# Performance work log

Hardware: AMD Instinct MI355X
Metric: run time of the kernel (lower is better)

## Reference

```python
import jax, jax.numpy as jnp
import numpy as np

N_NODES = 100000
N_EDGES = 1600000
D_IN = 64
D_OUT = 64


def _sage_conv(x, Wl, b, Wr, src, dst, inv_deg):
    # mean-aggregate neighbor features: gather x[src], scatter-sum into dst, divide by degree
    agg = jax.ops.segment_sum(x[src], dst, num_segments=N_NODES)  # [N, d]
    agg = agg * inv_deg                                            # mean with deg clamped >= 1
    # PyG SAGEConv: lin_l(agg) (with bias) + lin_r(x) (no bias)
    return agg @ Wl.T + b + x @ Wr.T


def setup_inputs() -> dict:
    key = jax.random.key(0)
    ks = jax.random.split(key, 8)
    x = jax.random.normal(ks[0], (N_NODES, D_IN), dtype=jnp.float32)
    edge_index = jax.random.randint(ks[1], (2, N_EDGES), 0, N_NODES, dtype=jnp.int64)
    s1 = 1.0 / np.sqrt(D_IN)
    s2 = 1.0 / np.sqrt(D_OUT)
    Wl1 = jax.random.uniform(ks[2], (D_OUT, D_IN), jnp.float32, -s1, s1)
    b1 = jnp.zeros((D_OUT,), jnp.float32)
    Wr1 = jax.random.uniform(ks[3], (D_OUT, D_IN), jnp.float32, -s1, s1)
    Wl2 = jax.random.uniform(ks[4], (D_OUT, D_OUT), jnp.float32, -s2, s2)
    b2 = jnp.zeros((D_OUT,), jnp.float32)
    Wr2 = jax.random.uniform(ks[5], (D_OUT, D_OUT), jnp.float32, -s2, s2)
    return {"x": x, "edge_index": edge_index, "Wl1": Wl1, "b1": b1, "Wr1": Wr1,
            "Wl2": Wl2, "b2": b2, "Wr2": Wr2}


def reference(x, edge_index, Wl1, b1, Wr1, Wl2, b2, Wr2):
    src, dst = edge_index[0], edge_index[1]
    deg = jax.ops.segment_sum(jnp.ones((N_EDGES,), jnp.float32), dst, num_segments=N_NODES)
    inv_deg = (1.0 / jnp.maximum(deg, 1.0))[:, None]  # [N, 1]
    h = _sage_conv(x, Wl1, b1, Wr1, src, dst, inv_deg)
    h = _sage_conv(h, Wl2, b2, Wr2, src, dst, inv_deg)
    return h
```

## Files before the change

### kernel.cpp

```cpp
#include <hip/hip_runtime.h>
#include <hip/hip_bf16.h>

#define NN 100000
#define NE 1600000
#define NB 196
#define BCAP 9216
#define BIN_CHUNK 8192
#define BIN_BLKS ((NE + BIN_CHUNK - 1) / BIN_CHUNK)

typedef __attribute__((ext_vector_type(8))) short bf16x8;
typedef __attribute__((ext_vector_type(4))) float f32x4;

__device__ inline unsigned short f2bf(float f) {
    union { __hip_bfloat16 h; unsigned short u; } c;
    c.h = __float2bfloat16(f);
    return c.u;
}

__global__ void k_init(int* __restrict__ gcur) {
    int t = threadIdx.x;
    if (t < NB) gcur[t] = t * BCAP;
}

__global__ void k_wcvt(const float* __restrict__ Wl1, const float* __restrict__ Wr1,
                       const float* __restrict__ Wl2, const float* __restrict__ Wr2,
                       unsigned short* __restrict__ Wc1, unsigned short* __restrict__ Wc2) {
    int e = blockIdx.x * 256 + threadIdx.x;
    if (e < 4096) {
        int fo = e >> 6, k = e & 63;
        Wc1[fo * 128 + k]      = f2bf(Wl1[e]);
        Wc1[fo * 128 + 64 + k] = f2bf(Wr1[e]);
        Wc2[fo * 128 + k]      = f2bf(Wl2[e]);
        Wc2[fo * 128 + 64 + k] = f2bf(Wr2[e]);
    }
}

__global__ __launch_bounds__(256) void k_xcvt(const float* __restrict__ x,
                                              unsigned short* __restrict__ xb) {
    int i = blockIdx.x * 256 + threadIdx.x;
    if (i >= NN * 64 / 8) return;
    const float4* p = (const float4*)(x + (size_t)i * 8);
    float4 v0 = p[0], v1 = p[1];
    union { bf16x8 v; unsigned short u[8]; } c;
    c.u[0] = f2bf(v0.x); c.u[1] = f2bf(v0.y); c.u[2] = f2bf(v0.z); c.u[3] = f2bf(v0.w);
    c.u[4] = f2bf(v1.x); c.u[5] = f2bf(v1.y); c.u[6] = f2bf(v1.z); c.u[7] = f2bf(v1.w);
    *(bf16x8*)(xb + (size_t)i * 8) = c.v;
}

__global__ __launch_bounds__(256) void k_bin(const int* __restrict__ src,
                                             const int* __restrict__ dst,
                                             int* __restrict__ gcur,
                                             unsigned* __restrict__ binned) {
    __shared__ int hist[NB];
    __shared__ int base[NB];
    __shared__ int lcur[NB];
    const int t = threadIdx.x;
    const int e0 = blockIdx.x * BIN_CHUNK;
    const int n = min(BIN_CHUNK, NE - e0);
    for (int i = t; i < NB; i += 256) { hist[i] = 0; lcur[i] = 0; }
    __syncthreads();
    for (int i = t; i < n; i += 256)
        atomicAdd(&hist[dst[e0 + i] >> 9], 1);
    __syncthreads();
    for (int i = t; i < NB; i += 256) {
        int h = hist[i];
        base[i] = h ? atomicAdd(&gcur[i], h) : 0;
    }
    __syncthreads();
    for (int i = t; i < n; i += 256) {
        int d = dst[e0 + i];
        int s = src[e0 + i];
        int b = d >> 9;
        int p = base[b] + atomicAdd(&lcur[b], 1);
        binned[p] = ((unsigned)(d & 511) << 17) | (unsigned)s;
    }
}

__global__ __launch_bounds__(256) void k_csr(const int* __restrict__ gcur,
                                             unsigned* __restrict__ binned,
                                             int2* __restrict__ noff,
                                             float* __restrict__ inv) {
    __shared__ unsigned buf[BCAP];
    __shared__ int h[512];
    __shared__ int off[512];
    __shared__ int lcur[512];
    __shared__ int s[256];
    const int b = blockIdx.x;
    const int t = threadIdx.x;
    const int base = b * BCAP;
    const int cnt = min(gcur[b] - base, BCAP);
    for (int i = t; i < 512; i += 256) h[i] = 0;
    __syncthreads();
    for (int i = t; i < cnt; i += 256) {
        unsigned v = binned[base + i];
        buf[i] = v;
        atomicAdd(&h[v >> 17], 1);
    }
    __syncthreads();
    int a0 = h[2 * t], a1 = h[2 * t + 1];
    s[t] = a0 + a1;
    __syncthreads();
    #pragma unroll
    for (int o = 1; o < 256; o <<= 1) {
        int u = (t >= o) ? s[t - o] : 0;
        __syncthreads();
        s[t] += u;
        __syncthreads();
    }
    int ex = s[t] - (a0 + a1);
    off[2 * t] = ex;          lcur[2 * t] = ex;
    off[2 * t + 1] = ex + a0; lcur[2 * t + 1] = ex + a0;
    __syncthreads();
    for (int i = t; i < cnt; i += 256) {
        unsigned v = buf[i];
        int dl = v >> 17;
        int p = atomicAdd(&lcur[dl], 1);
        binned[base + p] = v & 0x1FFFFu;
    }
    #pragma unroll
    for (int q = 0; q < 2; ++q) {
        int l = 2 * t + q;
        int node = b * 512 + l;
        if (node < NN) {
            int st = base + off[l];
            noff[node] = make_int2(st, st + h[l]);
            inv[node] = 1.0f / fmaxf((float)h[l], 1.0f);
        }
    }
}

__global__ __launch_bounds__(512) void k_agg(const unsigned short* __restrict__ feat,
                                             const int2* __restrict__ noff,
                                             const unsigned* __restrict__ csr,
                                             const float* __restrict__ inv,
                                             unsigned short* __restrict__ A) {
    int gid = (blockIdx.x * 512 + threadIdx.x) >> 3;
    int p = threadIdx.x & 7;
    if (gid >= NN) return;
    int2 oe = noff[gid];
    int beg = oe.x, end = oe.y;
    float a[8] = {0.f, 0.f, 0.f, 0.f, 0.f, 0.f, 0.f, 0.f};

    #define UNPK(uu, k)                                        \
        a[2*(k)]   += __uint_as_float((uu) << 16);             \
        a[2*(k)+1] += __uint_as_float((uu) & 0xffff0000u);

    int j = beg;
    for (; j + 4 <= end; j += 4) {
        unsigned s0 = csr[j], s1 = csr[j + 1], s2 = csr[j + 2], s3 = csr[j + 3];
        uint4 u0 = *(const uint4*)(feat + (size_t)s0 * 64 + p * 8);
        uint4 u1 = *(const uint4*)(feat + (size_t)s1 * 64 + p * 8);
        uint4 u2 = *(const uint4*)(feat + (size_t)s2 * 64 + p * 8);
        uint4 u3 = *(const uint4*)(feat + (size_t)s3 * 64 + p * 8);
        UNPK(u0.x, 0) UNPK(u0.y, 1) UNPK(u0.z, 2) UNPK(u0.w, 3)
        UNPK(u1.x, 0) UNPK(u1.y, 1) UNPK(u1.z, 2) UNPK(u1.w, 3)
        UNPK(u2.x, 0) UNPK(u2.y, 1) UNPK(u2.z, 2) UNPK(u2.w, 3)
        UNPK(u3.x, 0) UNPK(u3.y, 1) UNPK(u3.z, 2) UNPK(u3.w, 3)
    }
    for (; j < end; ++j) {
        uint4 u0 = *(const uint4*)(feat + (size_t)csr[j] * 64 + p * 8);
        UNPK(u0.x, 0) UNPK(u0.y, 1) UNPK(u0.z, 2) UNPK(u0.w, 3)
    }
    #undef UNPK

    float iv = inv[gid];
    union { bf16x8 v; unsigned short u[8]; } c;
    #pragma unroll
    for (int e = 0; e < 8; ++e) c.u[e] = f2bf(a[e] * iv);
    *(bf16x8*)(A + (size_t)gid * 64 + p * 8) = c.v;
}

__global__ __launch_bounds__(256) void k_gemm(const unsigned short* __restrict__ Ab,
                                              const unsigned short* __restrict__ Xb,
                                              const unsigned short* __restrict__ Wc,
                                              const float* __restrict__ bias,
                                              float* __restrict__ Cf,
                                              unsigned short* __restrict__ Cb) {
    const int t = threadIdx.x;
    const int w = t >> 6;
    const int l = t & 63;
    const int cn = l & 15;
    const int ks = l >> 4;
    const int n0 = blockIdx.x * 64 + w * 16;

    int arow = n0 + cn;
    int aclamp = (arow < NN) ? arow : 0;

    f32x4 acc0 = {0.f, 0.f, 0.f, 0.f};
    f32x4 acc1 = {0.f, 0.f, 0.f, 0.f};
    f32x4 acc2 = {0.f, 0.f, 0.f, 0.f};
    f32x4 acc3 = {0.f, 0.f, 0.f, 0.f};

    #pragma unroll
    for (int kb = 0; kb < 4; ++kb) {
        const unsigned short* ap = (kb < 2)
            ? (Ab + (size_t)aclamp * 64 + kb * 32 + ks * 8)
            : (Xb + (size_t)aclamp * 64 + (kb - 2) * 32 + ks * 8);
        bf16x8 aa = *(const bf16x8*)ap;
        const unsigned short* wb = Wc + cn * 128 + kb * 32 + ks * 8;
        bf16x8 b0 = *(const bf16x8*)(wb);
        bf16x8 b1 = *(const bf16x8*)(wb + 16 * 128);
        bf16x8 b2 = *(const bf16x8*)(wb + 32 * 128);
        bf16x8 b3 = *(const bf16x8*)(wb + 48 * 128);
        acc0 = __builtin_amdgcn_mfma_f32_16x16x32_bf16(aa, b0, acc0, 0, 0, 0);
        acc1 = __builtin_amdgcn_mfma_f32_16x16x32_bf16(aa, b1, acc1, 0, 0, 0);
        acc2 = __builtin_amdgcn_mfma_f32_16x16x32_bf16(aa, b2, acc2, 0, 0, 0);
        acc3 = __builtin_amdgcn_mfma_f32_16x16x32_bf16(aa, b3, acc3, 0, 0, 0);
    }

    #pragma unroll
    for (int f = 0; f < 4; ++f) {
        f32x4 av = (f == 0) ? acc0 : (f == 1) ? acc1 : (f == 2) ? acc2 : acc3;
        float bv = bias[f * 16 + cn];
        #pragma unroll
        for (int r = 0; r < 4; ++r) {
            int node = n0 + ks * 4 + r;
            if (node < NN) {
                float val = av[r] + bv;
                if (Cb) Cb[(size_t)node * 64 + f * 16 + cn] = f2bf(val);
                else    Cf[(size_t)node * 64 + f * 16 + cn] = val;
            }
        }
    }
}


extern "C" void kernel_launch(void* const* d_in, const int* in_sizes, int n_in,
                              void* d_out, int out_size, void* d_ws, size_t ws_size,
                              hipStream_t stream) {
    const float* x   = (const float*)d_in[0];
    const int*   ei  = (const int*)d_in[1];
    const int*   src = ei;
    const int*   dst = ei + NE;
    const float* Wl1 = (const float*)d_in[2];
    const float* b1  = (const float*)d_in[3];
    const float* Wr1 = (const float*)d_in[4];
    const float* Wl2 = (const float*)d_in[5];
    const float* b2  = (const float*)d_in[6];
    const float* Wr2 = (const float*)d_in[7];
    float* out = (float*)d_out;

    char* ws = (char*)d_ws;
    size_t off = 0;
    auto alloc = [&](size_t bytes) {
        void* p = ws + off;
        off = (off + bytes + 255) & ~(size_t)255;
        return p;
    };
    unsigned short* A      = (unsigned short*)alloc(2 * (size_t)NN * 64);
    unsigned short* xb     = (unsigned short*)alloc(2 * (size_t)NN * 64);
    unsigned short* h1b    = (unsigned short*)alloc(2 * (size_t)NN * 64);
    unsigned*       binned = (unsigned*)alloc(sizeof(unsigned) * NB * BCAP);
    int2*           noff   = (int2*)alloc(sizeof(int2) * NN);
    float*          inv    = (float*)alloc(sizeof(float) * NN);
    int*            gcur   = (int*)alloc(sizeof(int) * NB);
    unsigned short* Wc1    = (unsigned short*)alloc(2 * 64 * 128);
    unsigned short* Wc2    = (unsigned short*)alloc(2 * 64 * 128);

    k_init<<<1, 256, 0, stream>>>(gcur);
    k_wcvt<<<16, 256, 0, stream>>>(Wl1, Wr1, Wl2, Wr2, Wc1, Wc2);
    k_xcvt<<<(NN * 64 / 8 + 255) / 256, 256, 0, stream>>>(x, xb);
    k_bin <<<BIN_BLKS, 256, 0, stream>>>(src, dst, gcur, binned);
    k_csr <<<NB, 256, 0, stream>>>(gcur, binned, noff, inv);

    k_agg <<<((size_t)NN * 8 + 511) / 512, 512, 0, stream>>>(xb, noff, binned, inv, A);
    k_gemm<<<(NN + 63) / 64, 256, 0, stream>>>(A, xb, Wc1, b1, (float*)nullptr, h1b);

    k_agg <<<((size_t)NN * 8 + 511) / 512, 512, 0, stream>>>(h1b, noff, binned, inv, A);
    k_gemm<<<(NN + 63) / 64, 256, 0, stream>>>(A, h1b, Wc2, b2, out, (unsigned short*)nullptr);
}
```

Measured before the change: 165.4 us.

## Fuse aggregation with GEMM via shared memory and merge prep kernels

Each layer's aggregation and linear transform now run in one kernel. The mean-aggregated tile is written to LDS and fed straight into the MFMA, so the intermediate A buffer no longer makes a global round trip and one launch per layer is saved. The init, weight-convert and x-convert kernels are merged into a single prep kernel. The binning kernel also reads src and dst as int4. The GEMM work is split over 8 waves per 64-node block, each doing two output column groups.

```diff
diff --git a/kernel.cpp b/kernel.cpp
--- a/kernel.cpp
+++ b/kernel.cpp
@@ -17,34 +17,32 @@
     return c.u;
 }
 
-__global__ void k_init(int* __restrict__ gcur) {
-    int t = threadIdx.x;
-    if (t < NB) gcur[t] = t * BCAP;
-}
-
-__global__ void k_wcvt(const float* __restrict__ Wl1, const float* __restrict__ Wr1,
-                       const float* __restrict__ Wl2, const float* __restrict__ Wr2,
-                       unsigned short* __restrict__ Wc1, unsigned short* __restrict__ Wc2) {
-    int e = blockIdx.x * 256 + threadIdx.x;
-    if (e < 4096) {
-        int fo = e >> 6, k = e & 63;
-        Wc1[fo * 128 + k]      = f2bf(Wl1[e]);
-        Wc1[fo * 128 + 64 + k] = f2bf(Wr1[e]);
-        Wc2[fo * 128 + k]      = f2bf(Wl2[e]);
-        Wc2[fo * 128 + 64 + k] = f2bf(Wr2[e]);
-    }
-}
-
-__global__ __launch_bounds__(256) void k_xcvt(const float* __restrict__ x,
-                                              unsigned short* __restrict__ xb) {
+__global__ __launch_bounds__(256) void k_prep(const float* __restrict__ x,
+                                              unsigned short* __restrict__ xb,
+                                              const float* __restrict__ Wl1,
+                                              const float* __restrict__ Wr1,
+                                              const float* __restrict__ Wl2,
+                                              const float* __restrict__ Wr2,
+                                              unsigned short* __restrict__ Wc1,
+                                              unsigned short* __restrict__ Wc2,
+                                              int* __restrict__ gcur) {
     int i = blockIdx.x * 256 + threadIdx.x;
-    if (i >= NN * 64 / 8) return;
-    const float4* p = (const float4*)(x + (size_t)i * 8);
-    float4 v0 = p[0], v1 = p[1];
-    union { bf16x8 v; unsigned short u[8]; } c;
-    c.u[0] = f2bf(v0.x); c.u[1] = f2bf(v0.y); c.u[2] = f2bf(v0.z); c.u[3] = f2bf(v0.w);
-    c.u[4] = f2bf(v1.x); c.u[5] = f2bf(v1.y); c.u[6] = f2bf(v1.z); c.u[7] = f2bf(v1.w);
-    *(bf16x8*)(xb + (size_t)i * 8) = c.v;
+    if (i < NB) gcur[i] = i * BCAP;
+    if (i < 4096) {
+        int fo = i >> 6, k = i & 63;
+        Wc1[fo * 128 + k]      = f2bf(Wl1[i]);
+        Wc1[fo * 128 + 64 + k] = f2bf(Wr1[i]);
+        Wc2[fo * 128 + k]      = f2bf(Wl2[i]);
+        Wc2[fo * 128 + 64 + k] = f2bf(Wr2[i]);
+    }
+    if (i < NN * 64 / 8) {
+        const float4* p = (const float4*)(x + (size_t)i * 8);
+        float4 v0 = p[0], v1 = p[1];
+        union { bf16x8 v; unsigned short u[8]; } c;
+        c.u[0] = f2bf(v0.x); c.u[1] = f2bf(v0.y); c.u[2] = f2bf(v0.z); c.u[3] = f2bf(v0.w);
+        c.u[4] = f2bf(v1.x); c.u[5] = f2bf(v1.y); c.u[6] = f2bf(v1.z); c.u[7] = f2bf(v1.w);
+        *(bf16x8*)(xb + (size_t)i * 8) = c.v;
+    }
 }
 
 __global__ __launch_bounds__(256) void k_bin(const int* __restrict__ src,
@@ -56,23 +54,33 @@
     __shared__ int lcur[NB];
     const int t = threadIdx.x;
     const int e0 = blockIdx.x * BIN_CHUNK;
-    const int n = min(BIN_CHUNK, NE - e0);
+    const int n4 = min(BIN_CHUNK, NE - e0) >> 2;
     for (int i = t; i < NB; i += 256) { hist[i] = 0; lcur[i] = 0; }
     __syncthreads();
-    for (int i = t; i < n; i += 256)
-        atomicAdd(&hist[dst[e0 + i] >> 9], 1);
+    const int4* d4p = (const int4*)(dst + e0);
+    const int4* s4p = (const int4*)(src + e0);
+    for (int i = t; i < n4; i += 256) {
+        int4 d = d4p[i];
+        atomicAdd(&hist[d.x >> 9], 1);
+        atomicAdd(&hist[d.y >> 9], 1);
+        atomicAdd(&hist[d.z >> 9], 1);
+        atomicAdd(&hist[d.w >> 9], 1);
+    }
     __syncthreads();
     for (int i = t; i < NB; i += 256) {
         int h = hist[i];
         base[i] = h ? atomicAdd(&gcur[i], h) : 0;
     }
     __syncthreads();
-    for (int i = t; i < n; i += 256) {
-        int d = dst[e0 + i];
-        int s = src[e0 + i];
-        int b = d >> 9;
-        int p = base[b] + atomicAdd(&lcur[b], 1);
-        binned[p] = ((unsigned)(d & 511) << 17) | (unsigned)s;
+    for (int i = t; i < n4; i += 256) {
+        int4 d = d4p[i];
+        int4 s = s4p[i];
+        #define PLACE(dd, ss) {                                         \
+            int b = (dd) >> 9;                                          \
+            int p = base[b] + atomicAdd(&lcur[b], 1);                   \
+            binned[p] = ((unsigned)((dd) & 511) << 17) | (unsigned)(ss);}
+        PLACE(d.x, s.x) PLACE(d.y, s.y) PLACE(d.z, s.z) PLACE(d.w, s.w)
+        #undef PLACE
     }
 }
 
@@ -129,92 +137,91 @@
     }
 }
 
-__global__ __launch_bounds__(512) void k_agg(const unsigned short* __restrict__ feat,
-                                             const int2* __restrict__ noff,
-                                             const unsigned* __restrict__ csr,
-                                             const float* __restrict__ inv,
-                                             unsigned short* __restrict__ A) {
-    int gid = (blockIdx.x * 512 + threadIdx.x) >> 3;
-    int p = threadIdx.x & 7;
-    if (gid >= NN) return;
-    int2 oe = noff[gid];
-    int beg = oe.x, end = oe.y;
-    float a[8] = {0.f, 0.f, 0.f, 0.f, 0.f, 0.f, 0.f, 0.f};
-
-    #define UNPK(uu, k)                                        \
-        a[2*(k)]   += __uint_as_float((uu) << 16);             \
-        a[2*(k)+1] += __uint_as_float((uu) & 0xffff0000u);
-
-    int j = beg;
-    for (; j + 4 <= end; j += 4) {
-        unsigned s0 = csr[j], s1 = csr[j + 1], s2 = csr[j + 2], s3 = csr[j + 3];
-        uint4 u0 = *(const uint4*)(feat + (size_t)s0 * 64 + p * 8);
-        uint4 u1 = *(const uint4*)(feat + (size_t)s1 * 64 + p * 8);
-        uint4 u2 = *(const uint4*)(feat + (size_t)s2 * 64 + p * 8);
-        uint4 u3 = *(const uint4*)(feat + (size_t)s3 * 64 + p * 8);
-        UNPK(u0.x, 0) UNPK(u0.y, 1) UNPK(u0.z, 2) UNPK(u0.w, 3)
-        UNPK(u1.x, 0) UNPK(u1.y, 1) UNPK(u1.z, 2) UNPK(u1.w, 3)
-        UNPK(u2.x, 0) UNPK(u2.y, 1) UNPK(u2.z, 2) UNPK(u2.w, 3)
-        UNPK(u3.x, 0) UNPK(u3.y, 1) UNPK(u3.z, 2) UNPK(u3.w, 3)
-    }
-    for (; j < end; ++j) {
-        uint4 u0 = *(const uint4*)(feat + (size_t)csr[j] * 64 + p * 8);
-        UNPK(u0.x, 0) UNPK(u0.y, 1) UNPK(u0.z, 2) UNPK(u0.w, 3)
-    }
-    #undef UNPK
-
-    float iv = inv[gid];
-    union { bf16x8 v; unsigned short u[8]; } c;
-    #pragma unroll
-    for (int e = 0; e < 8; ++e) c.u[e] = f2bf(a[e] * iv);
-    *(bf16x8*)(A + (size_t)gid * 64 + p * 8) = c.v;
-}
-
-__global__ __launch_bounds__(256) void k_gemm(const unsigned short* __restrict__ Ab,
-                                              const unsigned short* __restrict__ Xb,
-                                              const unsigned short* __restrict__ Wc,
-                                              const float* __restrict__ bias,
-                                              float* __restrict__ Cf,
-                                              unsigned short* __restrict__ Cb) {
+__global__ __launch_bounds__(512) void k_fused(const unsigned short* __restrict__ feat,
+                                               const int2* __restrict__ noff,
+                                               const unsigned* __restrict__ csr,
+                                               const float* __restrict__ inv,
+                                               const unsigned short* __restrict__ Wc,
+                                               const float* __restrict__ bias,
+                                               float* __restrict__ Cf,
+                                               unsigned short* __restrict__ Cb) {
+    __shared__ unsigned short sA[64 * 72];
     const int t = threadIdx.x;
+    const int n0 = blockIdx.x * 64;
+
+    {
+        const int g = t >> 3;
+        const int p = t & 7;
+        const int node = n0 + g;
+        float a[8] = {0.f, 0.f, 0.f, 0.f, 0.f, 0.f, 0.f, 0.f};
+        float iv = 0.f;
+        if (node < NN) {
+            int2 oe = noff[node];
+            int beg = oe.x, end = oe.y;
+
+            #define UNPK(uu, k)                                        \
+                a[2*(k)]   += __uint_as_float((uu) << 16);             \
+                a[2*(k)+1] += __uint_as_float((uu) & 0xffff0000u);
+
+            int j = beg;
+            for (; j + 4 <= end; j += 4) {
+                unsigned s0 = csr[j], s1 = csr[j + 1], s2 = csr[j + 2], s3 = csr[j + 3];
+                uint4 u0 = *(const uint4*)(feat + (size_t)s0 * 64 + p * 8);
+                uint4 u1 = *(const uint4*)(feat + (size_t)s1 * 64 + p * 8);
+                uint4 u2 = *(const uint4*)(feat + (size_t)s2 * 64 + p * 8);
+                uint4 u3 = *(const uint4*)(feat + (size_t)s3 * 64 + p * 8);
+                UNPK(u0.x, 0) UNPK(u0.y, 1) UNPK(u0.z, 2) UNPK(u0.w, 3)
+                UNPK(u1.x, 0) UNPK(u1.y, 1) UNPK(u1.z, 2) UNPK(u1.w, 3)
+                UNPK(u2.x, 0) UNPK(u2.y, 1) UNPK(u2.z, 2) UNPK(u2.w, 3)
+                UNPK(u3.x, 0) UNPK(u3.y, 1) UNPK(u3.z, 2) UNPK(u3.w, 3)
+            }
+            for (; j < end; ++j) {
+                uint4 u0 = *(const uint4*)(feat + (size_t)csr[j] * 64 + p * 8);
+                UNPK(u0.x, 0) UNPK(u0.y, 1) UNPK(u0.z, 2) UNPK(u0.w, 3)
+            }
+            #undef UNPK
+            iv = inv[node];
+        }
+        union { bf16x8 v; unsigned short u[8]; } c;
+        #pragma unroll
+        for (int e = 0; e < 8; ++e) c.u[e] = f2bf(a[e] * iv);
+        *(bf16x8*)(&sA[g * 72 + p * 8]) = c.v;
+    }
+    __syncthreads();
+
     const int w = t >> 6;
     const int l = t & 63;
     const int cn = l & 15;
     const int ks = l >> 4;
-    const int n0 = blockIdx.x * 64 + w * 16;
-
-    int arow = n0 + cn;
-    int aclamp = (arow < NN) ? arow : 0;
+    const int s = w & 3;
+    const int h = w >> 2;
+    const int lrow = s * 16 + cn;
+    const int arow = n0 + lrow;
+    const int aclamp = (arow < NN) ? arow : 0;
 
     f32x4 acc0 = {0.f, 0.f, 0.f, 0.f};
     f32x4 acc1 = {0.f, 0.f, 0.f, 0.f};
-    f32x4 acc2 = {0.f, 0.f, 0.f, 0.f};
-    f32x4 acc3 = {0.f, 0.f, 0.f, 0.f};
 
     #pragma unroll
     for (int kb = 0; kb < 4; ++kb) {
-        const unsigned short* ap = (kb < 2)
-            ? (Ab + (size_t)aclamp * 64 + kb * 32 + ks * 8)
-            : (Xb + (size_t)aclamp * 64 + (kb - 2) * 32 + ks * 8);
-        bf16x8 aa = *(const bf16x8*)ap;
+        bf16x8 aa;
+        if (kb < 2) aa = *(const bf16x8*)(&sA[lrow * 72 + kb * 32 + ks * 8]);
+        else        aa = *(const bf16x8*)(feat + (size_t)aclamp * 64 + (kb - 2) * 32 + ks * 8);
         const unsigned short* wb = Wc + cn * 128 + kb * 32 + ks * 8;
-        bf16x8 b0 = *(const bf16x8*)(wb);
-        bf16x8 b1 = *(const bf16x8*)(wb + 16 * 128);
-        bf16x8 b2 = *(const bf16x8*)(wb + 32 * 128);
-        bf16x8 b3 = *(const bf16x8*)(wb + 48 * 128);
+        bf16x8 b0 = *(const bf16x8*)(wb + (size_t)(2 * h) * 16 * 128);
+        bf16x8 b1 = *(const bf16x8*)(wb + (size_t)(2 * h + 1) * 16 * 128);
         acc0 = __builtin_amdgcn_mfma_f32_16x16x32_bf16(aa, b0, acc0, 0, 0, 0);
         acc1 = __builtin_amdgcn_mfma_f32_16x16x32_bf16(aa, b1, acc1, 0, 0, 0);
-        acc2 = __builtin_amdgcn_mfma_f32_16x16x32_bf16(aa, b2, acc2, 0, 0, 0);
-        acc3 = __builtin_amdgcn_mfma_f32_16x16x32_bf16(aa, b3, acc3, 0, 0, 0);
-    }
-
-    #pragma unroll
-    for (int f = 0; f < 4; ++f) {
-        f32x4 av = (f == 0) ? acc0 : (f == 1) ? acc1 : (f == 2) ? acc2 : acc3;
+    }
+
+    #pragma unroll
+    for (int fb = 0; fb < 2; ++fb) {
+        f32x4 av = fb ? acc1 : acc0;
+        int f = 2 * h + fb;
         float bv = bias[f * 16 + cn];
         #pragma unroll
         for (int r = 0; r < 4; ++r) {
-            int node = n0 + ks * 4 + r;
+            int node = n0 + s * 16 + ks * 4 + r;
             if (node < NN) {
                 float val = av[r] + bv;
                 if (Cb) Cb[(size_t)node * 64 + f * 16 + cn] = f2bf(val);
@@ -247,7 +254,6 @@
         off = (off + bytes + 255) & ~(size_t)255;
         return p;
     };
-    unsigned short* A      = (unsigned short*)alloc(2 * (size_t)NN * 64);
     unsigned short* xb     = (unsigned short*)alloc(2 * (size_t)NN * 64);
     unsigned short* h1b    = (unsigned short*)alloc(2 * (size_t)NN * 64);
     unsigned*       binned = (unsigned*)alloc(sizeof(unsigned) * NB * BCAP);
@@ -257,15 +263,13 @@
     unsigned short* Wc1    = (unsigned short*)alloc(2 * 64 * 128);
     unsigned short* Wc2    = (unsigned short*)alloc(2 * 64 * 128);
 
-    k_init<<<1, 256, 0, stream>>>(gcur);
-    k_wcvt<<<16, 256, 0, stream>>>(Wl1, Wr1, Wl2, Wr2, Wc1, Wc2);
-    k_xcvt<<<(NN * 64 / 8 + 255) / 256, 256, 0, stream>>>(x, xb);
+    k_prep<<<(NN * 64 / 8 + 255) / 256, 256, 0, stream>>>(x, xb, Wl1, Wr1, Wl2, Wr2,
+                                                          Wc1, Wc2, gcur);
     k_bin <<<BIN_BLKS, 256, 0, stream>>>(src, dst, gcur, binned);
     k_csr <<<NB, 256, 0, stream>>>(gcur, binned, noff, inv);
 
-    k_agg <<<((size_t)NN * 8 + 511) / 512, 512, 0, stream>>>(xb, noff, binned, inv, A);
-    k_gemm<<<(NN + 63) / 64, 256, 0, stream>>>(A, xb, Wc1, b1, (float*)nullptr, h1b);
-
-    k_agg <<<((size_t)NN * 8 + 511) / 512, 512, 0, stream>>>(h1b, noff, binned, inv, A);
-    k_gemm<<<(NN + 63) / 64, 256, 0, stream>>>(A, h1b, Wc2, b2, out, (unsigned short*)nullptr);
-}
+    k_fused<<<(NN + 63) / 64, 512, 0, stream>>>(xb, noff, binned, inv, Wc1, b1,
+                                                (float*)nullptr, h1b);
+    k_fused<<<(NN + 63) / 64, 512, 0, stream>>>(h1b, noff, binned, inv, Wc2, b2,
+                                                out, (unsigned short*)nullptr);
+}
```

New measurement: 141.7 us. 1.17x faster.
